# Kernel tuning notes

Measured on AMD Instinct MI355X. Metric: run time of the kernel, lower is better.

## Reference

```python
import jax, jax.numpy as jnp
import numpy as np

B, EMBED, STATE, HIDDEN, HORIZON = 16384, 512, 128, 256, 32


def setup_inputs() -> dict:
    key = jax.random.key(0)
    ks = jax.random.split(key, 14)
    s = 0.05
    return {
        "embedding": jax.random.normal(ks[0], (B, EMBED), jnp.float32),
        "initial_state": jax.random.normal(ks[1], (B, STATE), jnp.float32),
        # input projection: embed_dim -> hidden_dim
        "Wp": jax.random.normal(ks[2], (HIDDEN, EMBED), jnp.float32) * s,
        "bp": jnp.zeros((HIDDEN,), jnp.float32),
        # GRU layer 0 (input = state_dim), gate order r,z,n as in PyTorch
        "Wih0": jax.random.normal(ks[3], (3 * HIDDEN, STATE), jnp.float32) * s,
        "Whh0": jax.random.normal(ks[4], (3 * HIDDEN, HIDDEN), jnp.float32) * s,
        "bih0": jax.random.normal(ks[5], (3 * HIDDEN,), jnp.float32) * s,
        "bhh0": jax.random.normal(ks[6], (3 * HIDDEN,), jnp.float32) * s,
        # GRU layer 1 (input = hidden_dim)
        "Wih1": jax.random.normal(ks[7], (3 * HIDDEN, HIDDEN), jnp.float32) * s,
        "Whh1": jax.random.normal(ks[8], (3 * HIDDEN, HIDDEN), jnp.float32) * s,
        "bih1": jax.random.normal(ks[9], (3 * HIDDEN,), jnp.float32) * s,
        "bhh1": jax.random.normal(ks[10], (3 * HIDDEN,), jnp.float32) * s,
        # output projection: hidden_dim -> state_dim
        "Wo": jax.random.normal(ks[11], (STATE, HIDDEN), jnp.float32) * s,
        "bo": jnp.zeros((STATE,), jnp.float32),
    }


def _gru_cell(x, h, Wih, Whh, bih, bhh):
    # PyTorch GRU cell: gates ordered (r, z, n)
    gi = x @ Wih.T + bih            # [B, 3H]
    gh = h @ Whh.T + bhh            # [B, 3H]
    ir, iz, inn = jnp.split(gi, 3, axis=-1)
    hr, hz, hn = jnp.split(gh, 3, axis=-1)
    r = jax.nn.sigmoid(ir + hr)
    z = jax.nn.sigmoid(iz + hz)
    n = jnp.tanh(inn + r * hn)
    return (1.0 - z) * n + z * h


def reference(embedding, initial_state, Wp, bp, Wih0, Whh0, bih0, bhh0,
              Wih1, Whh1, bih1, bhh1, Wo, bo):
    # Initial hidden for both GRU layers = projected embedding (repeated)
    h_init = embedding @ Wp.T + bp  # [B, H]

    def step(carry, _):
        h0, h1, state = carry
        h0 = _gru_cell(state, h0, Wih0, Whh0, bih0, bhh0)
        h1 = _gru_cell(h0, h1, Wih1, Whh1, bih1, bhh1)
        next_state = h1 @ Wo.T + bo  # [B, state_dim]
        return (h0, h1, next_state), next_state

    _, states = jax.lax.scan(step, (h_init, h_init, initial_state), None,
                             length=HORIZON)
    return jnp.transpose(states, (1, 0, 2))  # [B, horizon, state_dim]
```

## Files before the change

### kernel.cpp

```cpp
#include <hip/hip_runtime.h>


#define BTOT    16384
#define EMBED   512
#define STATE   128
#define HIDDEN  256
#define HORIZON 32

#define ROWS_PER_BLK 64
#define THREADS      512

typedef __attribute__((ext_vector_type(4))) float f32x4;
typedef __attribute__((ext_vector_type(8))) short s16x8;

#define N_Wp    (HIDDEN*EMBED)
#define N_Wih0  (3*HIDDEN*STATE)
#define N_Whh0  (3*HIDDEN*HIDDEN)
#define N_Wih1  (3*HIDDEN*HIDDEN)
#define N_Whh1  (3*HIDDEN*HIDDEN)
#define N_Wo    (STATE*HIDDEN)
#define OFF_Wp   0
#define OFF_Wih0 (OFF_Wp   + N_Wp)
#define OFF_Whh0 (OFF_Wih0 + N_Wih0)
#define OFF_Wih1 (OFF_Whh0 + N_Whh0)
#define OFF_Whh1 (OFF_Wih1 + N_Wih1)
#define OFF_Wo   (OFF_Whh1 + N_Whh1)
#define N_WTOT   (OFF_Wo   + N_Wo)

__device__ __forceinline__ short f2bf(float f) {
    unsigned u = __float_as_uint(f);
    u += 0x7FFFu + ((u >> 16) & 1u);
    return (short)(u >> 16);
}
__device__ __forceinline__ float bf2f(short h) {
    return __uint_as_float(((unsigned)(unsigned short)h) << 16);
}
__device__ __forceinline__ void split8(const f32x4 a, const f32x4 b, s16x8 &hi, s16x8 &lo) {
#pragma unroll
    for (int i = 0; i < 4; i++) {
        short h = f2bf(a[i]); hi[i] = h; lo[i] = f2bf(a[i] - bf2f(h));
    }
#pragma unroll
    for (int i = 0; i < 4; i++) {
        short h = f2bf(b[i]); hi[4+i] = h; lo[4+i] = f2bf(b[i] - bf2f(h));
    }
}

__device__ __forceinline__ int swz(int row, int col, int stride) {
    return row * stride + ((((col >> 2) ^ (row & 7)) << 2) | (col & 3));
}

template<int STRIDE>
__device__ __forceinline__ void lds_frag(const float* H, int row, int k0, s16x8 &hi, s16x8 &lo) {
    int base = row * STRIDE;
    int s0 = (((k0 >> 2)    ) ^ (row & 7)) << 2;
    int s1 = (((k0 >> 2) + 1) ^ (row & 7)) << 2;
    f32x4 a = *(const f32x4*)(H + base + s0);
    f32x4 b = *(const f32x4*)(H + base + s1);
    split8(a, b, hi, lo);
}
__device__ __forceinline__ void glob_frag(const float* __restrict__ S, int row, int k0,
                                          s16x8 &hi, s16x8 &lo) {
    f32x4 a = *(const f32x4*)(S + (size_t)row * STATE + k0);
    f32x4 b = *(const f32x4*)(S + (size_t)row * STATE + k0 + 4);
    split8(a, b, hi, lo);
}

#define MFMA(A, B, C) __builtin_amdgcn_mfma_f32_16x16x32_bf16(A, B, C, 0, 0, 0)

template<int KW>
__device__ __forceinline__ void catblock(f32x4 (&acc)[4],
                                         const s16x8 (&ahi)[4], const s16x8 (&alo)[4],
                                         const short* __restrict__ WHi,
                                         const short* __restrict__ WLo,
                                         int wr, int k0) {
    s16x8 bhi = *(const s16x8*)(WHi + wr * KW + k0);
    s16x8 blo = *(const s16x8*)(WLo + wr * KW + k0);
#pragma unroll
    for (int mt = 0; mt < 4; mt++) acc[mt] = MFMA(ahi[mt], bhi, acc[mt]);
#pragma unroll
    for (int mt = 0; mt < 4; mt++) acc[mt] = MFMA(alo[mt], bhi, acc[mt]);
#pragma unroll
    for (int mt = 0; mt < 4; mt++) acc[mt] = MFMA(ahi[mt], blo, acc[mt]);
}

__device__ __forceinline__ float sigf(float x)  { return 1.0f / (1.0f + __expf(-x)); }
__device__ __forceinline__ float tanhf_(float x){ return 1.0f - 2.0f / (__expf(2.0f * x) + 1.0f); }

template<int KI, bool AGLOB>
__device__ __forceinline__ void gru_layer(
    const float* __restrict__ Ai,
    const float* __restrict__ Hlds,
    const short* __restrict__ WihHi, const short* __restrict__ WihLo,
    const short* __restrict__ WhhHi, const short* __restrict__ WhhLo,
    const float* __restrict__ bih,   const float* __restrict__ bhh,
    int rowbase, int wave, int lr, int lg,
    float hnew[2][4][4])
{
#pragma unroll
    for (int p = 0; p < 2; p++) {
        f32x4 aR[4], aZ[4], aI[4], aH[4];
        {
            f32x4 zz = {0.f, 0.f, 0.f, 0.f};
#pragma unroll
            for (int mt = 0; mt < 4; mt++) { aR[mt]=zz; aZ[mt]=zz; aI[mt]=zz; aH[mt]=zz; }
        }
        const int hcol = wave * 32 + p * 16 + lr;
#pragma unroll 2
        for (int kc = 0; kc < KI / 32; kc++) {
            const int k0 = kc * 32 + lg * 8;
            s16x8 ahi[4], alo[4];
#pragma unroll
            for (int mt = 0; mt < 4; mt++) {
                if constexpr (AGLOB) glob_frag(Ai, rowbase + mt * 16 + lr, k0, ahi[mt], alo[mt]);
                else                 lds_frag<KI>(Ai, mt * 16 + lr, k0, ahi[mt], alo[mt]);
            }
            catblock<KI>(aR, ahi, alo, WihHi, WihLo, 0 * HIDDEN + hcol, k0);
            catblock<KI>(aZ, ahi, alo, WihHi, WihLo, 1 * HIDDEN + hcol, k0);
            catblock<KI>(aI, ahi, alo, WihHi, WihLo, 2 * HIDDEN + hcol, k0);
        }
#pragma unroll 2
        for (int kc = 0; kc < HIDDEN / 32; kc++) {
            const int k0 = kc * 32 + lg * 8;
            s16x8 ahi[4], alo[4];
#pragma unroll
            for (int mt = 0; mt < 4; mt++)
                lds_frag<HIDDEN>(Hlds, mt * 16 + lr, k0, ahi[mt], alo[mt]);
            catblock<HIDDEN>(aR, ahi, alo, WhhHi, WhhLo, 0 * HIDDEN + hcol, k0);
            catblock<HIDDEN>(aZ, ahi, alo, WhhHi, WhhLo, 1 * HIDDEN + hcol, k0);
            catblock<HIDDEN>(aH, ahi, alo, WhhHi, WhhLo, 2 * HIDDEN + hcol, k0);
        }
        const float b_r = bih[hcol]            + bhh[hcol];
        const float b_z = bih[HIDDEN + hcol]   + bhh[HIDDEN + hcol];
        const float b_i = bih[2 * HIDDEN + hcol];
        const float b_h = bhh[2 * HIDDEN + hcol];
#pragma unroll
        for (int mt = 0; mt < 4; mt++)
#pragma unroll
            for (int j = 0; j < 4; j++) {
                int row  = mt * 16 + lg * 4 + j;
                float r  = sigf(aR[mt][j] + b_r);
                float z  = sigf(aZ[mt][j] + b_z);
                float n  = tanhf_(aI[mt][j] + b_i + r * (aH[mt][j] + b_h));
                float ho = Hlds[swz(row, hcol, HIDDEN)];
                hnew[p][mt][j] = (1.0f - z) * n + z * ho;
            }
    }
}

__device__ __forceinline__ void write_h(float* Hlds, const float hnew[2][4][4],
                                        int wave, int lr, int lg) {
#pragma unroll
    for (int p = 0; p < 2; p++) {
        int col = wave * 32 + p * 16 + lr;
#pragma unroll
        for (int mt = 0; mt < 4; mt++)
#pragma unroll
            for (int j = 0; j < 4; j++)
                Hlds[swz(mt * 16 + lg * 4 + j, col, HIDDEN)] = hnew[p][mt][j];
    }
}

__global__ void prep_split(const float* __restrict__ Wp,   const float* __restrict__ Wih0,
                           const float* __restrict__ Whh0, const float* __restrict__ Wih1,
                           const float* __restrict__ Whh1, const float* __restrict__ Wo,
                           short* __restrict__ hi, short* __restrict__ lo) {
    int i = blockIdx.x * 256 + threadIdx.x;
    if (i >= N_WTOT) return;
    float w;
    if      (i < OFF_Wih0) w = Wp  [i - OFF_Wp];
    else if (i < OFF_Whh0) w = Wih0[i - OFF_Wih0];
    else if (i < OFF_Wih1) w = Whh0[i - OFF_Whh0];
    else if (i < OFF_Whh1) w = Wih1[i - OFF_Wih1];
    else if (i < OFF_Wo)   w = Whh1[i - OFF_Whh1];
    else                   w = Wo  [i - OFF_Wo];
    short h = f2bf(w);
    hi[i] = h;
    lo[i] = f2bf(w - bf2f(h));
}

__global__ __launch_bounds__(THREADS, 2)
void gru_main(const float* __restrict__ emb,  const float* __restrict__ init_state,
              const float* __restrict__ bp,
              const float* __restrict__ bih0, const float* __restrict__ bhh0,
              const float* __restrict__ bih1, const float* __restrict__ bhh1,
              const float* __restrict__ bo,
              const short* __restrict__ Whi,  const short* __restrict__ Wlo,
              float* __restrict__ wsS, float* __restrict__ out) {
    __shared__ float smem[ROWS_PER_BLK * EMBED];
    float* H0 = smem;
    float* H1 = smem + ROWS_PER_BLK * HIDDEN;

    const int tid  = threadIdx.x;
    const int wave = tid >> 6, lane = tid & 63;
    const int lr = lane & 15, lg = lane >> 4;
    const int rowbase = blockIdx.x * ROWS_PER_BLK;

    const short *WpHi   = Whi + OFF_Wp,   *WpLo   = Wlo + OFF_Wp;
    const short *Wih0Hi = Whi + OFF_Wih0, *Wih0Lo = Wlo + OFF_Wih0;
    const short *Whh0Hi = Whi + OFF_Whh0, *Whh0Lo = Wlo + OFF_Whh0;
    const short *Wih1Hi = Whi + OFF_Wih1, *Wih1Lo = Wlo + OFF_Wih1;
    const short *Whh1Hi = Whi + OFF_Whh1, *Whh1Lo = Wlo + OFF_Whh1;
    const short *WoHi   = Whi + OFF_Wo,   *WoLo   = Wlo + OFF_Wo;

    for (int idx = tid; idx < ROWS_PER_BLK * EMBED; idx += THREADS) {
        int r = idx >> 9, c = idx & (EMBED - 1);
        smem[swz(r, c, EMBED)] = emb[(size_t)(rowbase + r) * EMBED + c];
    }
    __syncthreads();
    f32x4 hacc[2][4];
    {
        f32x4 zz = {0.f, 0.f, 0.f, 0.f};
#pragma unroll
        for (int nt = 0; nt < 2; nt++)
#pragma unroll
            for (int mt = 0; mt < 4; mt++) hacc[nt][mt] = zz;
    }
#pragma unroll 2
    for (int kc = 0; kc < EMBED / 32; kc++) {
        const int k0 = kc * 32 + lg * 8;
        s16x8 ahi[4], alo[4];
#pragma unroll
        for (int mt = 0; mt < 4; mt++)
            lds_frag<EMBED>(smem, mt * 16 + lr, k0, ahi[mt], alo[mt]);
#pragma unroll
        for (int nt = 0; nt < 2; nt++)
            catblock<EMBED>(hacc[nt], ahi, alo, WpHi, WpLo, wave * 32 + nt * 16 + lr, k0);
    }
    __syncthreads();
#pragma unroll
    for (int nt = 0; nt < 2; nt++)
#pragma unroll
        for (int mt = 0; mt < 4; mt++)
#pragma unroll
            for (int j = 0; j < 4; j++) {
                int row = mt * 16 + lg * 4 + j;
                int col = wave * 32 + nt * 16 + lr;
                float v = hacc[nt][mt][j] + bp[col];
                H0[swz(row, col, HIDDEN)] = v;
                H1[swz(row, col, HIDDEN)] = v;
            }
    __syncthreads();

    for (int t = 0; t < HORIZON; t++) {
        const float* Srd = (t == 0) ? init_state : wsS;

        float hn0[2][4][4];
        gru_layer<STATE, true>(Srd, H0, Wih0Hi, Wih0Lo, Whh0Hi, Whh0Lo,
                               bih0, bhh0, rowbase, wave, lr, lg, hn0);
        __syncthreads();
        write_h(H0, hn0, wave, lr, lg);
        __syncthreads();

        float hn1[2][4][4];
        gru_layer<HIDDEN, false>(H0, H1, Wih1Hi, Wih1Lo, Whh1Hi, Whh1Lo,
                                 bih1, bhh1, rowbase, wave, lr, lg, hn1);
        __syncthreads();
        write_h(H1, hn1, wave, lr, lg);
        __syncthreads();

        f32x4 o[4];
        {
            f32x4 zz = {0.f, 0.f, 0.f, 0.f};
#pragma unroll
            for (int mt = 0; mt < 4; mt++) o[mt] = zz;
        }
#pragma unroll 2
        for (int kc = 0; kc < HIDDEN / 32; kc++) {
            const int k0 = kc * 32 + lg * 8;
            s16x8 ahi[4], alo[4];
#pragma unroll
            for (int mt = 0; mt < 4; mt++)
                lds_frag<HIDDEN>(H1, mt * 16 + lr, k0, ahi[mt], alo[mt]);
            catblock<HIDDEN>(o, ahi, alo, WoHi, WoLo, wave * 16 + lr, k0);
        }
        const int scol = wave * 16 + lr;
        const float bov = bo[scol];
#pragma unroll
        for (int mt = 0; mt < 4; mt++)
#pragma unroll
            for (int j = 0; j < 4; j++) {
                int row   = mt * 16 + lg * 4 + j;
                size_t gr = (size_t)(rowbase + row);
                float v   = o[mt][j] + bov;
                out[gr * (size_t)(HORIZON * STATE) + (size_t)t * STATE + scol] = v;
                wsS[gr * STATE + scol] = v;
            }
        __threadfence_block();
        __syncthreads();
    }
}

extern "C" void kernel_launch(void* const* d_in, const int* in_sizes, int n_in,
                              void* d_out, int out_size, void* d_ws, size_t ws_size,
                              hipStream_t stream) {
    (void)in_sizes; (void)n_in; (void)out_size; (void)ws_size;
    const float* emb  = (const float*)d_in[0];
    const float* st0  = (const float*)d_in[1];
    const float* Wp   = (const float*)d_in[2];
    const float* bp   = (const float*)d_in[3];
    const float* Wih0 = (const float*)d_in[4];
    const float* Whh0 = (const float*)d_in[5];
    const float* bih0 = (const float*)d_in[6];
    const float* bhh0 = (const float*)d_in[7];
    const float* Wih1 = (const float*)d_in[8];
    const float* Whh1 = (const float*)d_in[9];
    const float* bih1 = (const float*)d_in[10];
    const float* bhh1 = (const float*)d_in[11];
    const float* Wo   = (const float*)d_in[12];
    const float* bo   = (const float*)d_in[13];
    float* out = (float*)d_out;

    float* wsS = (float*)d_ws;
    short* whi = (short*)((char*)d_ws + (size_t)BTOT * STATE * sizeof(float));
    short* wlo = whi + N_WTOT;

    prep_split<<<(N_WTOT + 255) / 256, 256, 0, stream>>>(Wp, Wih0, Whh0, Wih1, Whh1, Wo, whi, wlo);
    gru_main<<<BTOT / ROWS_PER_BLK, THREADS, 0, stream>>>(
        emb, st0, bp, bih0, bhh0, bih1, bhh1, bo, whi, wlo, wsS, out);
}
```

Measured before the change: 5.695 ms.

## Store hidden and state activations as pre-split bf16 hi/lo pairs

Hidden states in LDS and the recurrent state in the global workspace are now stored as bf16 hi/lo pairs instead of fp32. The hi/lo split then happens once per write, not on every fragment load inside the MFMA loops. The LDS swizzle moves to 8-element granularity so each fragment is a single 16-byte load. Bias values are hoisted into registers before the time loop, and a new kernel pre-splits the initial state. The cost is extra conversion work on every write and two loads (hi and lo) to rebuild the previous hidden value.

```diff
diff --git a/kernel.cpp b/kernel.cpp
--- a/kernel.cpp
+++ b/kernel.cpp
@@ -46,23 +46,23 @@
     }
 }
 
-__device__ __forceinline__ int swz(int row, int col, int stride) {
-    return row * stride + ((((col >> 2) ^ (row & 7)) << 2) | (col & 3));
-}
-
-template<int STRIDE>
-__device__ __forceinline__ void lds_frag(const float* H, int row, int k0, s16x8 &hi, s16x8 &lo) {
-    int base = row * STRIDE;
+__device__ __forceinline__ int sidx(int row, int col) {
+    return row * 256 + ((((col >> 3) ^ (row & 7)) << 3) | (col & 7));
+}
+__device__ __forceinline__ int sfrag(int row, int k0) {
+    return row * 256 + (((k0 >> 3) ^ (row & 7)) << 3);
+}
+
+__device__ __forceinline__ int fswz(int row, int col) {
+    return row * EMBED + ((((col >> 2) ^ (row & 7)) << 2) | (col & 3));
+}
+__device__ __forceinline__ void lds_frag_f32(const float* H, int row, int k0,
+                                             s16x8 &hi, s16x8 &lo) {
+    int base = row * EMBED;
     int s0 = (((k0 >> 2)    ) ^ (row & 7)) << 2;
     int s1 = (((k0 >> 2) + 1) ^ (row & 7)) << 2;
     f32x4 a = *(const f32x4*)(H + base + s0);
     f32x4 b = *(const f32x4*)(H + base + s1);
-    split8(a, b, hi, lo);
-}
-__device__ __forceinline__ void glob_frag(const float* __restrict__ S, int row, int k0,
-                                          s16x8 &hi, s16x8 &lo) {
-    f32x4 a = *(const f32x4*)(S + (size_t)row * STATE + k0);
-    f32x4 b = *(const f32x4*)(S + (size_t)row * STATE + k0 + 4);
     split8(a, b, hi, lo);
 }
 
@@ -89,11 +89,11 @@
 
 template<int KI, bool AGLOB>
 __device__ __forceinline__ void gru_layer(
-    const float* __restrict__ Ai,
-    const float* __restrict__ Hlds,
+    const short* __restrict__ AiHi, const short* __restrict__ AiLo,
+    const short* __restrict__ HHi,  const short* __restrict__ HLo,
     const short* __restrict__ WihHi, const short* __restrict__ WihLo,
     const short* __restrict__ WhhHi, const short* __restrict__ WhhLo,
-    const float* __restrict__ bih,   const float* __restrict__ bhh,
+    const float br[2], const float bz[2], const float bi[2], const float bh[2],
     int rowbase, int wave, int lr, int lg,
     float hnew[2][4][4])
 {
@@ -112,8 +112,15 @@
             s16x8 ahi[4], alo[4];
 #pragma unroll
             for (int mt = 0; mt < 4; mt++) {
-                if constexpr (AGLOB) glob_frag(Ai, rowbase + mt * 16 + lr, k0, ahi[mt], alo[mt]);
-                else                 lds_frag<KI>(Ai, mt * 16 + lr, k0, ahi[mt], alo[mt]);
+                if constexpr (AGLOB) {
+                    size_t base = (size_t)(rowbase + mt * 16 + lr) * KI + k0;
+                    ahi[mt] = *(const s16x8*)(AiHi + base);
+                    alo[mt] = *(const s16x8*)(AiLo + base);
+                } else {
+                    int off = sfrag(mt * 16 + lr, k0);
+                    ahi[mt] = *(const s16x8*)(AiHi + off);
+                    alo[mt] = *(const s16x8*)(AiLo + off);
+                }
             }
             catblock<KI>(aR, ahi, alo, WihHi, WihLo, 0 * HIDDEN + hcol, k0);
             catblock<KI>(aZ, ahi, alo, WihHi, WihLo, 1 * HIDDEN + hcol, k0);
@@ -124,31 +131,30 @@
             const int k0 = kc * 32 + lg * 8;
             s16x8 ahi[4], alo[4];
 #pragma unroll
-            for (int mt = 0; mt < 4; mt++)
-                lds_frag<HIDDEN>(Hlds, mt * 16 + lr, k0, ahi[mt], alo[mt]);
+            for (int mt = 0; mt < 4; mt++) {
+                int off = sfrag(mt * 16 + lr, k0);
+                ahi[mt] = *(const s16x8*)(HHi + off);
+                alo[mt] = *(const s16x8*)(HLo + off);
+            }
             catblock<HIDDEN>(aR, ahi, alo, WhhHi, WhhLo, 0 * HIDDEN + hcol, k0);
             catblock<HIDDEN>(aZ, ahi, alo, WhhHi, WhhLo, 1 * HIDDEN + hcol, k0);
             catblock<HIDDEN>(aH, ahi, alo, WhhHi, WhhLo, 2 * HIDDEN + hcol, k0);
         }
-        const float b_r = bih[hcol]            + bhh[hcol];
-        const float b_z = bih[HIDDEN + hcol]   + bhh[HIDDEN + hcol];
-        const float b_i = bih[2 * HIDDEN + hcol];
-        const float b_h = bhh[2 * HIDDEN + hcol];
 #pragma unroll
         for (int mt = 0; mt < 4; mt++)
 #pragma unroll
             for (int j = 0; j < 4; j++) {
                 int row  = mt * 16 + lg * 4 + j;
-                float r  = sigf(aR[mt][j] + b_r);
-                float z  = sigf(aZ[mt][j] + b_z);
-                float n  = tanhf_(aI[mt][j] + b_i + r * (aH[mt][j] + b_h));
-                float ho = Hlds[swz(row, hcol, HIDDEN)];
+                float r  = sigf(aR[mt][j] + br[p]);
+                float z  = sigf(aZ[mt][j] + bz[p]);
+                float n  = tanhf_(aI[mt][j] + bi[p] + r * (aH[mt][j] + bh[p]));
+                float ho = bf2f(HHi[sidx(row, hcol)]) + bf2f(HLo[sidx(row, hcol)]);
                 hnew[p][mt][j] = (1.0f - z) * n + z * ho;
             }
     }
 }
 
-__device__ __forceinline__ void write_h(float* Hlds, const float hnew[2][4][4],
+__device__ __forceinline__ void write_h(short* HHi, short* HLo, const float hnew[2][4][4],
                                         int wave, int lr, int lg) {
 #pragma unroll
     for (int p = 0; p < 2; p++) {
@@ -156,8 +162,14 @@
 #pragma unroll
         for (int mt = 0; mt < 4; mt++)
 #pragma unroll
-            for (int j = 0; j < 4; j++)
-                Hlds[swz(mt * 16 + lg * 4 + j, col, HIDDEN)] = hnew[p][mt][j];
+            for (int j = 0; j < 4; j++) {
+                int row = mt * 16 + lg * 4 + j;
+                float v = hnew[p][mt][j];
+                short hi = f2bf(v);
+                short lo = f2bf(v - bf2f(hi));
+                HHi[sidx(row, col)] = hi;
+                HLo[sidx(row, col)] = lo;
+            }
     }
 }
 
@@ -179,17 +191,31 @@
     lo[i] = f2bf(w - bf2f(h));
 }
 
+__global__ void prep_state(const float* __restrict__ s0,
+                           short* __restrict__ shi, short* __restrict__ slo) {
+    int i = blockIdx.x * 256 + threadIdx.x;
+    if (i >= BTOT * STATE) return;
+    float w = s0[i];
+    short h = f2bf(w);
+    shi[i] = h;
+    slo[i] = f2bf(w - bf2f(h));
+}
+
 __global__ __launch_bounds__(THREADS, 2)
-void gru_main(const float* __restrict__ emb,  const float* __restrict__ init_state,
+void gru_main(const float* __restrict__ emb,
               const float* __restrict__ bp,
               const float* __restrict__ bih0, const float* __restrict__ bhh0,
               const float* __restrict__ bih1, const float* __restrict__ bhh1,
               const float* __restrict__ bo,
               const short* __restrict__ Whi,  const short* __restrict__ Wlo,
-              float* __restrict__ wsS, float* __restrict__ out) {
-    __shared__ float smem[ROWS_PER_BLK * EMBED];
-    float* H0 = smem;
-    float* H1 = smem + ROWS_PER_BLK * HIDDEN;
+              short* __restrict__ Shi, short* __restrict__ Slo,
+              float* __restrict__ out) {
+    __shared__ short sH[4 * ROWS_PER_BLK * HIDDEN];
+    short* H0hi = sH;
+    short* H0lo = sH + 1 * ROWS_PER_BLK * HIDDEN;
+    short* H1hi = sH + 2 * ROWS_PER_BLK * HIDDEN;
+    short* H1lo = sH + 3 * ROWS_PER_BLK * HIDDEN;
+    float* fl   = (float*)sH;
 
     const int tid  = threadIdx.x;
     const int wave = tid >> 6, lane = tid & 63;
@@ -203,9 +229,29 @@
     const short *Whh1Hi = Whi + OFF_Whh1, *Whh1Lo = Wlo + OFF_Whh1;
     const short *WoHi   = Whi + OFF_Wo,   *WoLo   = Wlo + OFF_Wo;
 
+    float br0[2], bz0[2], bi0[2], bh0[2];
+    float br1[2], bz1[2], bi1[2], bh1[2];
+#pragma unroll
+    for (int p = 0; p < 2; p++) {
+        int c = wave * 32 + p * 16 + lr;
+        br0[p] = bih0[c] + bhh0[c];
+        bz0[p] = bih0[HIDDEN + c] + bhh0[HIDDEN + c];
+        bi0[p] = bih0[2 * HIDDEN + c];
+        bh0[p] = bhh0[2 * HIDDEN + c];
+        br1[p] = bih1[c] + bhh1[c];
+        bz1[p] = bih1[HIDDEN + c] + bhh1[HIDDEN + c];
+        bi1[p] = bih1[2 * HIDDEN + c];
+        bh1[p] = bhh1[2 * HIDDEN + c];
+    }
+    const int scol = wave * 16 + lr;
+    const float bo_v = bo[scol];
+    float bpv[2];
+    bpv[0] = bp[wave * 32 + lr];
+    bpv[1] = bp[wave * 32 + 16 + lr];
+
     for (int idx = tid; idx < ROWS_PER_BLK * EMBED; idx += THREADS) {
         int r = idx >> 9, c = idx & (EMBED - 1);
-        smem[swz(r, c, EMBED)] = emb[(size_t)(rowbase + r) * EMBED + c];
+        fl[fswz(r, c)] = emb[(size_t)(rowbase + r) * EMBED + c];
     }
     __syncthreads();
     f32x4 hacc[2][4];
@@ -222,7 +268,7 @@
         s16x8 ahi[4], alo[4];
 #pragma unroll
         for (int mt = 0; mt < 4; mt++)
-            lds_frag<EMBED>(smem, mt * 16 + lr, k0, ahi[mt], alo[mt]);
+            lds_frag_f32(fl, mt * 16 + lr, k0, ahi[mt], alo[mt]);
 #pragma unroll
         for (int nt = 0; nt < 2; nt++)
             catblock<EMBED>(hacc[nt], ahi, alo, WpHi, WpLo, wave * 32 + nt * 16 + lr, k0);
@@ -236,27 +282,32 @@
             for (int j = 0; j < 4; j++) {
                 int row = mt * 16 + lg * 4 + j;
                 int col = wave * 32 + nt * 16 + lr;
-                float v = hacc[nt][mt][j] + bp[col];
-                H0[swz(row, col, HIDDEN)] = v;
-                H1[swz(row, col, HIDDEN)] = v;
+                float v = hacc[nt][mt][j] + bpv[nt];
+                short hi = f2bf(v);
+                short lo = f2bf(v - bf2f(hi));
+                H0hi[sidx(row, col)] = hi;  H0lo[sidx(row, col)] = lo;
+                H1hi[sidx(row, col)] = hi;  H1lo[sidx(row, col)] = lo;
             }
     __syncthreads();
 
+#pragma unroll 1
     for (int t = 0; t < HORIZON; t++) {
-        const float* Srd = (t == 0) ? init_state : wsS;
-
         float hn0[2][4][4];
-        gru_layer<STATE, true>(Srd, H0, Wih0Hi, Wih0Lo, Whh0Hi, Whh0Lo,
-                               bih0, bhh0, rowbase, wave, lr, lg, hn0);
-        __syncthreads();
-        write_h(H0, hn0, wave, lr, lg);
+        gru_layer<STATE, true>(Shi, Slo, H0hi, H0lo,
+                               Wih0Hi, Wih0Lo, Whh0Hi, Whh0Lo,
+                               br0, bz0, bi0, bh0,
+                               rowbase, wave, lr, lg, hn0);
+        __syncthreads();
+        write_h(H0hi, H0lo, hn0, wave, lr, lg);
         __syncthreads();
 
         float hn1[2][4][4];
-        gru_layer<HIDDEN, false>(H0, H1, Wih1Hi, Wih1Lo, Whh1Hi, Whh1Lo,
-                                 bih1, bhh1, rowbase, wave, lr, lg, hn1);
-        __syncthreads();
-        write_h(H1, hn1, wave, lr, lg);
+        gru_layer<HIDDEN, false>(H0hi, H0lo, H1hi, H1lo,
+                                 Wih1Hi, Wih1Lo, Whh1Hi, Whh1Lo,
+                                 br1, bz1, bi1, bh1,
+                                 rowbase, wave, lr, lg, hn1);
+        __syncthreads();
+        write_h(H1hi, H1lo, hn1, wave, lr, lg);
         __syncthreads();
 
         f32x4 o[4];
@@ -270,21 +321,25 @@
             const int k0 = kc * 32 + lg * 8;
             s16x8 ahi[4], alo[4];
 #pragma unroll
-            for (int mt = 0; mt < 4; mt++)
-                lds_frag<HIDDEN>(H1, mt * 16 + lr, k0, ahi[mt], alo[mt]);
-            catblock<HIDDEN>(o, ahi, alo, WoHi, WoLo, wave * 16 + lr, k0);
-        }
-        const int scol = wave * 16 + lr;
-        const float bov = bo[scol];
+            for (int mt = 0; mt < 4; mt++) {
+                int off = sfrag(mt * 16 + lr, k0);
+                ahi[mt] = *(const s16x8*)(H1hi + off);
+                alo[mt] = *(const s16x8*)(H1lo + off);
+            }
+            catblock<HIDDEN>(o, ahi, alo, WoHi, WoLo, scol, k0);
+        }
 #pragma unroll
         for (int mt = 0; mt < 4; mt++)
 #pragma unroll
             for (int j = 0; j < 4; j++) {
                 int row   = mt * 16 + lg * 4 + j;
                 size_t gr = (size_t)(rowbase + row);
-                float v   = o[mt][j] + bov;
+                float v   = o[mt][j] + bo_v;
                 out[gr * (size_t)(HORIZON * STATE) + (size_t)t * STATE + scol] = v;
-                wsS[gr * STATE + scol] = v;
+                short hi = f2bf(v);
+                short lo = f2bf(v - bf2f(hi));
+                Shi[gr * STATE + scol] = hi;
+                Slo[gr * STATE + scol] = lo;
             }
         __threadfence_block();
         __syncthreads();
@@ -311,11 +366,13 @@
     const float* bo   = (const float*)d_in[13];
     float* out = (float*)d_out;
 
-    float* wsS = (float*)d_ws;
-    short* whi = (short*)((char*)d_ws + (size_t)BTOT * STATE * sizeof(float));
+    short* shi = (short*)d_ws;
+    short* slo = shi + (size_t)BTOT * STATE;
+    short* whi = slo + (size_t)BTOT * STATE;
     short* wlo = whi + N_WTOT;
 
     prep_split<<<(N_WTOT + 255) / 256, 256, 0, stream>>>(Wp, Wih0, Whh0, Wih1, Whh1, Wo, whi, wlo);
+    prep_state<<<(BTOT * STATE + 255) / 256, 256, 0, stream>>>(st0, shi, slo);
     gru_main<<<BTOT / ROWS_PER_BLK, THREADS, 0, stream>>>(
-        emb, st0, bp, bih0, bhh0, bih1, bhh1, bo, whi, wlo, wsS, out);
-}
+        emb, bp, bih0, bhh0, bih1, bhh1, bo, whi, wlo, shi, slo, out);
+}
```

Result: no change. 5.611 ms (-1.5%).
